# Optimization experiments

Hardware: AMD Instinct MI355X
Metric: run time of the kernel (lower is better)

Reference implementation:

```python
import jax, jax.numpy as jnp
import numpy as np
from jax import lax

MAXV = 8      # convex intersection of two quads has at most 8 vertices
EPS = 1e-7
LOSS_WEIGHT = 1.0


def _edge_cross(A, B, P):
    # z of (B-A) x (P-A); >= 0 means P is on the left of directed edge A->B (inside for CCW poly)
    return (B[0] - A[0]) * (P[1] - A[1]) - (B[1] - A[1]) * (P[0] - A[0])


def _clip_halfplane(pts, n, A, B):
    # Sutherland-Hodgman clip of polygon pts[:n] against left halfplane of edge A->B.
    # pts: (MAXV,2) buffer, n: traced vertex count. Returns new buffer + count.
    def body(i, carry):
        out, m = carry
        valid = i < n
        cur = pts[i]
        nxt = pts[jnp.mod(i + 1, jnp.maximum(n, 1))]
        dc = _edge_cross(A, B, cur)
        dn = _edge_cross(A, B, nxt)
        denom = dc - dn
        t = dc / jnp.where(jnp.abs(denom) < EPS, 1.0, denom)
        ip = cur + t * (nxt - cur)
        add_cur = valid & (dc >= 0)
        idx = jnp.minimum(m, MAXV - 1)
        out = jnp.where(add_cur, out.at[idx].set(cur), out)
        m = m + add_cur.astype(jnp.int32)
        add_ip = valid & jnp.logical_xor(dc >= 0, dn >= 0)
        idx = jnp.minimum(m, MAXV - 1)
        out = jnp.where(add_ip, out.at[idx].set(ip), out)
        m = m + add_ip.astype(jnp.int32)
        return out, m
    out0 = jnp.zeros((MAXV, 2), pts.dtype)
    return lax.fori_loop(0, MAXV, body, (out0, jnp.int32(0)))


def _shoelace_masked(pts, n):
    # signed area of pts[:n] (fixed-size loop, masked)
    def body(i, acc):
        valid = i < n
        cur = pts[i]
        nxt = pts[jnp.mod(i + 1, jnp.maximum(n, 1))]
        term = cur[0] * nxt[1] - cur[1] * nxt[0]
        return acc + jnp.where(valid, term, jnp.zeros((), pts.dtype))
    return 0.5 * lax.fori_loop(0, MAXV, body, jnp.zeros((), pts.dtype))


def _quad_signed_area(p):  # p: (4,2)
    x, y = p[:, 0], p[:, 1]
    return 0.5 * jnp.sum(x * jnp.roll(y, -1) - y * jnp.roll(x, -1))


def _diou_single(p, t):
    # p, t: (4,2) quads -> scalar poly DIoU loss (a=0 => standard DIoU penalty)
    sa_p = _quad_signed_area(p)
    sa_t = _quad_signed_area(t)
    p = jnp.where(sa_p < 0, p[::-1], p)   # force CCW orientation
    t = jnp.where(sa_t < 0, t[::-1], t)
    area_p = jnp.abs(sa_p)
    area_t = jnp.abs(sa_t)
    # clip p by the 4 halfplanes of t
    buf = jnp.zeros((MAXV, 2), p.dtype).at[:4].set(p)
    n = jnp.int32(4)
    for k in range(4):
        buf, n = _clip_halfplane(buf, n, t[k], t[(k + 1) % 4])
    inter = jnp.abs(_shoelace_masked(buf, n))
    union = area_p + area_t - inter
    iou = inter / (union + EPS)
    cp = p.mean(0)
    ct = t.mean(0)
    d2 = jnp.sum((cp - ct) ** 2)
    allp = jnp.concatenate([p, t], axis=0)
    c2 = jnp.sum((allp.max(0) - allp.min(0)) ** 2) + EPS
    return 1.0 - iou + d2 / c2


def setup_inputs() -> dict:
    key = jax.random.key(0)
    k1, k2 = jax.random.split(key)
    N = 2_000_000
    pred = jax.random.uniform(k1, (N, 8), dtype=jnp.float32)
    target = jax.random.uniform(k2, (N, 8), dtype=jnp.float32)
    return {"pred": pred, "target": target}


def reference(pred, target):
    p = pred.reshape(-1, 4, 2)
    t = target.reshape(-1, 4, 2)
    losses = jax.vmap(_diou_single)(p, t)  # (N,)
    return LOSS_WEIGHT * losses.mean()
```

## Files before the change

### kernel.cpp

```cpp
#include <hip/hip_runtime.h>

#define NBLOCKS 2048
#define NTHREADS 256
#define FEPS 1e-7f

__device__ __forceinline__ float frcp(float x) { return __builtin_amdgcn_rcpf(x); }

__device__ __forceinline__ int clip1_to_lds(float2* base,
                                            const float (&px)[4], const float (&py)[4],
                                            float Ax, float Ay, float ex, float ey) {
    float c[4];
#pragma unroll
    for (int j = 0; j < 4; ++j)
        c[j] = ex * (py[j] - Ay) - ey * (px[j] - Ax);
    int m = 0;
#pragma unroll
    for (int i = 0; i < 4; ++i) {
        int ip1 = (i + 1) & 3;
        float dc = c[i], dn = c[ip1];
        float nx = px[ip1], ny = py[ip1];
        float denom = dc - dn;
        float d = (fabsf(denom) < FEPS) ? 1.0f : denom;
        float t = dc * frcp(d);
        float ipx = px[i] + t * (nx - px[i]);
        float ipy = py[i] + t * (ny - py[i]);
        bool sc = dc >= 0.0f, sn = dn >= 0.0f;

        bool add_cur = sc;
        int i1 = add_cur ? ((m < 7) ? m : 7) : 8;
        base[i1 * NTHREADS] = make_float2(px[i], py[i]);
        m += add_cur ? 1 : 0;

        bool add_ip = (sc != sn);
        int i2 = add_ip ? ((m < 7) ? m : 7) : 8;
        base[i2 * NTHREADS] = make_float2(ipx, ipy);
        m += add_ip ? 1 : 0;
    }
    return m;
}

__device__ __forceinline__ int clip_lds(float2* base, int n,
                                        float Ax, float Ay, float ex, float ey) {
    float vx[8], vy[8], c[8];
#pragma unroll
    for (int j = 0; j < 8; ++j) {
        float2 v = base[j * NTHREADS];
        vx[j] = v.x; vy[j] = v.y;
    }
#pragma unroll
    for (int j = 0; j < 8; ++j)
        c[j] = ex * (vy[j] - Ay) - ey * (vx[j] - Ax);
    int m = 0;
#pragma unroll
    for (int i = 0; i < 8; ++i) {
        bool valid = i < n;
        bool wrap = (i + 1 == n);
        int ip1 = (i < 7) ? (i + 1) : 7;
        float nx = wrap ? vx[0] : vx[ip1];
        float ny = wrap ? vy[0] : vy[ip1];
        float dc = c[i];
        float dn = wrap ? c[0] : c[ip1];
        float denom = dc - dn;
        float d = (fabsf(denom) < FEPS) ? 1.0f : denom;
        float t = dc * frcp(d);
        float ipx = vx[i] + t * (nx - vx[i]);
        float ipy = vy[i] + t * (ny - vy[i]);
        bool sc = dc >= 0.0f, sn = dn >= 0.0f;

        bool add_cur = valid && sc;
        int i1 = add_cur ? ((m < 7) ? m : 7) : 8;
        base[i1 * NTHREADS] = make_float2(vx[i], vy[i]);
        m += add_cur ? 1 : 0;

        bool add_ip = valid && (sc != sn);
        int i2 = add_ip ? ((m < 7) ? m : 7) : 8;
        base[i2 * NTHREADS] = make_float2(ipx, ipy);
        m += add_ip ? 1 : 0;
    }
    return m;
}

__device__ __forceinline__ float diou_quad(float2* base,
                                           float4 pa, float4 pb, float4 ta, float4 tb) {
    float px[4] = {pa.x, pa.z, pb.x, pb.z};
    float py[4] = {pa.y, pa.w, pb.y, pb.w};
    float tx[4] = {ta.x, ta.z, tb.x, tb.z};
    float ty[4] = {ta.y, ta.w, tb.y, tb.w};

    float sa_p = 0.5f * ((px[0] * py[1] - py[0] * px[1]) +
                         (px[1] * py[2] - py[1] * px[2]) +
                         (px[2] * py[3] - py[2] * px[3]) +
                         (px[3] * py[0] - py[3] * px[0]));
    float sa_t = 0.5f * ((tx[0] * ty[1] - ty[0] * tx[1]) +
                         (tx[1] * ty[2] - ty[1] * tx[2]) +
                         (tx[2] * ty[3] - ty[2] * tx[3]) +
                         (tx[3] * ty[0] - ty[3] * tx[0]));

    if (sa_p < 0.0f) {
        float t0;
        t0 = px[0]; px[0] = px[3]; px[3] = t0;
        t0 = px[1]; px[1] = px[2]; px[2] = t0;
        t0 = py[0]; py[0] = py[3]; py[3] = t0;
        t0 = py[1]; py[1] = py[2]; py[2] = t0;
    }
    if (sa_t < 0.0f) {
        float t0;
        t0 = tx[0]; tx[0] = tx[3]; tx[3] = t0;
        t0 = tx[1]; tx[1] = tx[2]; tx[2] = t0;
        t0 = ty[0]; ty[0] = ty[3]; ty[3] = t0;
        t0 = ty[1]; ty[1] = ty[2]; ty[2] = t0;
    }
    float area_p = fabsf(sa_p);
    float area_t = fabsf(sa_t);

    int n = clip1_to_lds(base, px, py, tx[0], ty[0], tx[1] - tx[0], ty[1] - ty[0]);
    n = clip_lds(base, n, tx[1], ty[1], tx[2] - tx[1], ty[2] - ty[1]);
    n = clip_lds(base, n, tx[2], ty[2], tx[3] - tx[2], ty[3] - ty[2]);
    n = clip_lds(base, n, tx[3], ty[3], tx[0] - tx[3], ty[0] - ty[3]);

    float vx[8], vy[8];
#pragma unroll
    for (int j = 0; j < 8; ++j) {
        float2 v = base[j * NTHREADS];
        vx[j] = v.x; vy[j] = v.y;
    }
    float acc = 0.0f;
#pragma unroll
    for (int i = 0; i < 8; ++i) {
        bool valid = i < n;
        bool wrap = (i + 1 == n);
        int ip1 = (i < 7) ? (i + 1) : 7;
        float nx = wrap ? vx[0] : vx[ip1];
        float ny = wrap ? vy[0] : vy[ip1];
        float term = vx[i] * ny - vy[i] * nx;
        acc += valid ? term : 0.0f;
    }
    float inter = fabsf(0.5f * acc);
    float uni = area_p + area_t - inter;
    float iou = inter * frcp(uni + FEPS);

    float cpx = 0.25f * (px[0] + px[1] + px[2] + px[3]);
    float cpy = 0.25f * (py[0] + py[1] + py[2] + py[3]);
    float ctx = 0.25f * (tx[0] + tx[1] + tx[2] + tx[3]);
    float cty = 0.25f * (ty[0] + ty[1] + ty[2] + ty[3]);
    float d2 = (cpx - ctx) * (cpx - ctx) + (cpy - cty) * (cpy - cty);

    float minx = fminf(fminf(fminf(px[0], px[1]), fminf(px[2], px[3])),
                       fminf(fminf(tx[0], tx[1]), fminf(tx[2], tx[3])));
    float maxx = fmaxf(fmaxf(fmaxf(px[0], px[1]), fmaxf(px[2], px[3])),
                       fmaxf(fmaxf(tx[0], tx[1]), fmaxf(tx[2], tx[3])));
    float miny = fminf(fminf(fminf(py[0], py[1]), fminf(py[2], py[3])),
                       fminf(fminf(ty[0], ty[1]), fminf(ty[2], ty[3])));
    float maxy = fmaxf(fmaxf(fmaxf(py[0], py[1]), fmaxf(py[2], py[3])),
                       fmaxf(fmaxf(ty[0], ty[1]), fmaxf(ty[2], ty[3])));
    float c2 = (maxx - minx) * (maxx - minx) + (maxy - miny) * (maxy - miny) + FEPS;

    return 1.0f - iou + d2 * frcp(c2);
}

__global__ __launch_bounds__(NTHREADS) void diou_main(const float* __restrict__ pred,
                                                      const float* __restrict__ target,
                                                      double* __restrict__ partial,
                                                      int N) {
    __shared__ float2 poly[9 * NTHREADS];
    __shared__ double wsum[NTHREADS / 64];
    float2* base = &poly[threadIdx.x];

    const float4* p4 = reinterpret_cast<const float4*>(pred);
    const float4* t4 = reinterpret_cast<const float4*>(target);

    double acc = 0.0;
    for (int i = blockIdx.x * NTHREADS + threadIdx.x; i < N; i += NBLOCKS * NTHREADS) {
        float4 pa = p4[2 * i], pb = p4[2 * i + 1];
        float4 ta = t4[2 * i], tb = t4[2 * i + 1];
        acc += (double)diou_quad(base, pa, pb, ta, tb);
    }

#pragma unroll
    for (int off = 32; off > 0; off >>= 1) acc += __shfl_down(acc, off, 64);
    int lane = threadIdx.x & 63, wid = threadIdx.x >> 6;
    if (lane == 0) wsum[wid] = acc;
    __syncthreads();
    if (threadIdx.x == 0) {
        double s = 0.0;
#pragma unroll
        for (int w = 0; w < NTHREADS / 64; ++w) s += wsum[w];
        partial[blockIdx.x] = s;
    }
}

__global__ __launch_bounds__(256) void diou_finalize(const double* __restrict__ partial,
                                                     float* __restrict__ out,
                                                     int nparts, double invN) {
    __shared__ double s[256];
    double acc = 0.0;
    for (int i = threadIdx.x; i < nparts; i += 256) acc += partial[i];
    s[threadIdx.x] = acc;
    __syncthreads();
#pragma unroll
    for (int off = 128; off > 0; off >>= 1) {
        if (threadIdx.x < off) s[threadIdx.x] += s[threadIdx.x + off];
        __syncthreads();
    }
    if (threadIdx.x == 0) out[0] = (float)(s[0] * invN);
}

extern "C" void kernel_launch(void* const* d_in, const int* in_sizes, int n_in,
                              void* d_out, int out_size, void* d_ws, size_t ws_size,
                              hipStream_t stream) {
    const float* pred = (const float*)d_in[0];
    const float* target = (const float*)d_in[1];
    float* out = (float*)d_out;
    int N = in_sizes[0] / 8;

    double* partial = (double*)d_ws;

    diou_main<<<NBLOCKS, NTHREADS, 0, stream>>>(pred, target, partial, N);
    diou_finalize<<<1, 256, 0, stream>>>(partial, out, NBLOCKS, 1.0 / (double)N);
}
```

Before: 57.65 us.

## Skip wave-uniform empty clip iterations, precompute edge offsets, add occupancy hint

Each edge's line offset is precomputed so the cross product becomes two FMAs, and the intersection lerps are written as FMAs. In the clip and shoelace loops, iterations from index 4 onward break early when no lane in the wave has that many vertices. The index clamps are dropped where the count cannot yet exceed 7, and a min-blocks-per-CU hint of 6 is added to launch bounds. The wave vote adds a branch and may limit unrolling. Folding the offset into the cross product changes float rounding slightly.

```diff
diff --git a/kernel.cpp b/kernel.cpp
--- a/kernel.cpp
+++ b/kernel.cpp
@@ -8,54 +8,53 @@
 
 __device__ __forceinline__ int clip1_to_lds(float2* base,
                                             const float (&px)[4], const float (&py)[4],
-                                            float Ax, float Ay, float ex, float ey) {
+                                            float ex, float ey, float h) {
     float c[4];
 #pragma unroll
     for (int j = 0; j < 4; ++j)
-        c[j] = ex * (py[j] - Ay) - ey * (px[j] - Ax);
+        c[j] = fmaf(ex, py[j], -fmaf(ey, px[j], h));
     int m = 0;
 #pragma unroll
     for (int i = 0; i < 4; ++i) {
-        int ip1 = (i + 1) & 3;
+        const int ip1 = (i + 1) & 3;
         float dc = c[i], dn = c[ip1];
         float nx = px[ip1], ny = py[ip1];
         float denom = dc - dn;
         float d = (fabsf(denom) < FEPS) ? 1.0f : denom;
         float t = dc * frcp(d);
-        float ipx = px[i] + t * (nx - px[i]);
-        float ipy = py[i] + t * (ny - py[i]);
+        float ipx = fmaf(t, nx - px[i], px[i]);
+        float ipy = fmaf(t, ny - py[i], py[i]);
         bool sc = dc >= 0.0f, sn = dn >= 0.0f;
 
         bool add_cur = sc;
-        int i1 = add_cur ? ((m < 7) ? m : 7) : 8;
+        int i1 = add_cur ? m : 8;
         base[i1 * NTHREADS] = make_float2(px[i], py[i]);
-        m += add_cur ? 1 : 0;
+        m += add_cur;
 
         bool add_ip = (sc != sn);
-        int i2 = add_ip ? ((m < 7) ? m : 7) : 8;
+        int i2 = add_ip ? m : 8;
         base[i2 * NTHREADS] = make_float2(ipx, ipy);
-        m += add_ip ? 1 : 0;
+        m += add_ip;
     }
     return m;
 }
 
 __device__ __forceinline__ int clip_lds(float2* base, int n,
-                                        float Ax, float Ay, float ex, float ey) {
+                                        float ex, float ey, float h) {
     float vx[8], vy[8], c[8];
 #pragma unroll
     for (int j = 0; j < 8; ++j) {
         float2 v = base[j * NTHREADS];
         vx[j] = v.x; vy[j] = v.y;
-    }
-#pragma unroll
-    for (int j = 0; j < 8; ++j)
-        c[j] = ex * (vy[j] - Ay) - ey * (vx[j] - Ax);
+        c[j] = fmaf(ex, vy[j], -fmaf(ey, vx[j], h));
+    }
     int m = 0;
 #pragma unroll
     for (int i = 0; i < 8; ++i) {
+        if (i >= 4 && !__any(i < n)) break;
         bool valid = i < n;
         bool wrap = (i + 1 == n);
-        int ip1 = (i < 7) ? (i + 1) : 7;
+        const int ip1 = (i < 7) ? (i + 1) : 7;
         float nx = wrap ? vx[0] : vx[ip1];
         float ny = wrap ? vy[0] : vy[ip1];
         float dc = c[i];
@@ -63,19 +62,23 @@
         float denom = dc - dn;
         float d = (fabsf(denom) < FEPS) ? 1.0f : denom;
         float t = dc * frcp(d);
-        float ipx = vx[i] + t * (nx - vx[i]);
-        float ipy = vy[i] + t * (ny - vy[i]);
+        float ipx = fmaf(t, nx - vx[i], vx[i]);
+        float ipy = fmaf(t, ny - vy[i], vy[i]);
         bool sc = dc >= 0.0f, sn = dn >= 0.0f;
 
         bool add_cur = valid && sc;
-        int i1 = add_cur ? ((m < 7) ? m : 7) : 8;
+        int i1;
+        if (i < 4) i1 = add_cur ? m : 8;
+        else       i1 = add_cur ? ((m < 7) ? m : 7) : 8;
         base[i1 * NTHREADS] = make_float2(vx[i], vy[i]);
-        m += add_cur ? 1 : 0;
+        m += add_cur;
 
         bool add_ip = valid && (sc != sn);
-        int i2 = add_ip ? ((m < 7) ? m : 7) : 8;
+        int i2;
+        if (i < 4) i2 = add_ip ? m : 8;
+        else       i2 = add_ip ? ((m < 7) ? m : 7) : 8;
         base[i2 * NTHREADS] = make_float2(ipx, ipy);
-        m += add_ip ? 1 : 0;
+        m += add_ip;
     }
     return m;
 }
@@ -113,10 +116,23 @@
     float area_p = fabsf(sa_p);
     float area_t = fabsf(sa_t);
 
-    int n = clip1_to_lds(base, px, py, tx[0], ty[0], tx[1] - tx[0], ty[1] - ty[0]);
-    n = clip_lds(base, n, tx[1], ty[1], tx[2] - tx[1], ty[2] - ty[1]);
-    n = clip_lds(base, n, tx[2], ty[2], tx[3] - tx[2], ty[3] - ty[2]);
-    n = clip_lds(base, n, tx[3], ty[3], tx[0] - tx[3], ty[0] - ty[3]);
+    int n;
+    {
+        float ex = tx[1] - tx[0], ey = ty[1] - ty[0];
+        n = clip1_to_lds(base, px, py, ex, ey, fmaf(ex, ty[0], -ey * tx[0]));
+    }
+    {
+        float ex = tx[2] - tx[1], ey = ty[2] - ty[1];
+        n = clip_lds(base, n, ex, ey, fmaf(ex, ty[1], -ey * tx[1]));
+    }
+    {
+        float ex = tx[3] - tx[2], ey = ty[3] - ty[2];
+        n = clip_lds(base, n, ex, ey, fmaf(ex, ty[2], -ey * tx[2]));
+    }
+    {
+        float ex = tx[0] - tx[3], ey = ty[0] - ty[3];
+        n = clip_lds(base, n, ex, ey, fmaf(ex, ty[3], -ey * tx[3]));
+    }
 
     float vx[8], vy[8];
 #pragma unroll
@@ -127,9 +143,10 @@
     float acc = 0.0f;
 #pragma unroll
     for (int i = 0; i < 8; ++i) {
+        if (i >= 4 && !__any(i < n)) break;
         bool valid = i < n;
         bool wrap = (i + 1 == n);
-        int ip1 = (i < 7) ? (i + 1) : 7;
+        const int ip1 = (i < 7) ? (i + 1) : 7;
         float nx = wrap ? vx[0] : vx[ip1];
         float ny = wrap ? vy[0] : vy[ip1];
         float term = vx[i] * ny - vy[i] * nx;
@@ -158,10 +175,10 @@
     return 1.0f - iou + d2 * frcp(c2);
 }
 
-__global__ __launch_bounds__(NTHREADS) void diou_main(const float* __restrict__ pred,
-                                                      const float* __restrict__ target,
-                                                      double* __restrict__ partial,
-                                                      int N) {
+__global__ __launch_bounds__(NTHREADS, 6) void diou_main(const float* __restrict__ pred,
+                                                         const float* __restrict__ target,
+                                                         double* __restrict__ partial,
+                                                         int N) {
     __shared__ float2 poly[9 * NTHREADS];
     __shared__ double wsum[NTHREADS / 64];
     float2* base = &poly[threadIdx.x];
```

After: 50.42 us. -12.5%, faster.
